# Kernel optimization log

Hardware: AMD Instinct MI355X
Metric: run time of the kernel (lower is better)

Reference implementation:

```python
import jax, jax.numpy as jnp
import numpy as np

N = 200000      # nodes
E = 12_800_000  # edges
G = 512         # graphs in batch
D = 2           # point_dim


def setup_inputs() -> dict:
    key = jax.random.key(0)
    ks = jax.random.split(key, 12)
    x = jax.random.normal(ks[0], (N, D), dtype=jnp.float32)
    edge_index = jax.random.randint(ks[1], (2, E), 0, N, dtype=jnp.int64)
    batch = jnp.sort(jax.random.randint(ks[2], (N,), 0, G, dtype=jnp.int64))
    s = 0.5
    W1 = jax.random.normal(ks[3], (D, 2), dtype=jnp.float32) * s
    b1 = jax.random.normal(ks[4], (2,), dtype=jnp.float32) * 0.1
    W2 = jax.random.normal(ks[5], (2, 2), dtype=jnp.float32) * s
    b2 = jax.random.normal(ks[6], (2,), dtype=jnp.float32) * 0.1
    W3 = jax.random.normal(ks[7], (2, 2), dtype=jnp.float32) * s
    b3 = jax.random.normal(ks[8], (2,), dtype=jnp.float32) * 0.1
    Wr = jax.random.normal(ks[9], (2, 1), dtype=jnp.float32) * s
    br = jax.random.normal(ks[10], (1,), dtype=jnp.float32) * 0.1
    return {"x": x, "edge_index": edge_index, "batch": batch,
            "W1": W1, "b1": b1, "W2": W2, "b2": b2,
            "W3": W3, "b3": b3, "Wr": Wr, "br": br}


def _gcn_conv(x, W, b, src, dst, norm, n_nodes):
    # PyG GCNConv: h = x @ W; out_i = sum_j norm_ij * h_j (incl. self-loops) + b
    h = x @ W
    agg = jax.ops.segment_sum(h[src] * norm[:, None], dst, num_segments=n_nodes)
    return agg + b


def reference(x, edge_index, batch, W1, b1, W2, b2, W3, b3, Wr, br):
    n = x.shape[0]
    loop = jnp.arange(n, dtype=edge_index.dtype)
    # GCNConv adds self-loops; same edge_index for all layers, so do it once.
    src = jnp.concatenate([edge_index[0], loop])
    dst = jnp.concatenate([edge_index[1], loop])
    # symmetric normalization: deg from target nodes (incl self-loops)
    deg = jax.ops.segment_sum(jnp.ones(dst.shape[0], x.dtype), dst, num_segments=n)
    dinv = jnp.where(deg > 0, jax.lax.rsqrt(deg), 0.0)
    norm = dinv[src] * dinv[dst]

    h = jax.nn.relu(_gcn_conv(x, W1, b1, src, dst, norm, n))
    h = jax.nn.relu(_gcn_conv(h, W2, b2, src, dst, norm, n))
    h = jax.nn.relu(_gcn_conv(h, W3, b3, src, dst, norm, n))
    pooled = jax.ops.segment_sum(h, batch, num_segments=G)  # global_add_pool -> [G, 2]
    return (pooled @ Wr + br)[:, 0]  # squeeze(1) -> [G]
```

## Files before the change

### kernel.cpp

```cpp
#include <hip/hip_runtime.h>

#define BLK 256
#define BLK2 1024
#define BSHIFT 8
#define BSIZE 256
#define NSLICE 256
#define SCAN_T 1024
#define KPAD 1024
#define EPT 8
#define TILE (BLK * EPT)
#define TILE2 (BLK2 * EPT)

typedef int iv4 __attribute__((ext_vector_type(4)));

template <typename T>
__device__ __forceinline__ T ntload(const T* p) { return __builtin_nontemporal_load(p); }

__device__ __forceinline__ iv4 ntload4(const int* p) {
    return __builtin_nontemporal_load((const iv4*)p);
}

template <int CTRL>
__device__ __forceinline__ float dpp_add(float v) {
    int t = __builtin_amdgcn_update_dpp(0, __float_as_int(v), CTRL, 0xf, 0xf, true);
    return v + __int_as_float(t);
}
__device__ __forceinline__ float wave_sum63(float v) {
    v = dpp_add<0x111>(v);
    v = dpp_add<0x112>(v);
    v = dpp_add<0x114>(v);
    v = dpp_add<0x118>(v);
    v = dpp_add<0x142>(v);
    v = dpp_add<0x143>(v);
    return v;
}


__global__ void __launch_bounds__(BLK2) k_hist(const int* __restrict__ dst,
                                               int* __restrict__ partial,
                                               int E, int chunk, int K) {
    extern __shared__ int cnt[];
    int s = blockIdx.x;
    for (int i = threadIdx.x; i < K; i += BLK2) cnt[i] = 0;
    __syncthreads();
    int lo = s * chunk, hi = min(E, lo + chunk);
    int a0 = min((lo + 3) & ~3, hi);
    int a1 = max(hi & ~3, a0);
    for (int i = lo + threadIdx.x; i < a0; i += BLK2)
        atomicAdd(&cnt[((unsigned)ntload(dst + i)) >> BSHIFT], 1);
    for (int i = a0 + 4 * threadIdx.x; i < a1; i += 4 * BLK2) {
        iv4 q = ntload4(dst + i);
        atomicAdd(&cnt[((unsigned)q.x) >> BSHIFT], 1);
        atomicAdd(&cnt[((unsigned)q.y) >> BSHIFT], 1);
        atomicAdd(&cnt[((unsigned)q.z) >> BSHIFT], 1);
        atomicAdd(&cnt[((unsigned)q.w) >> BSHIFT], 1);
    }
    for (int i = a1 + threadIdx.x; i < hi; i += BLK2)
        atomicAdd(&cnt[((unsigned)ntload(dst + i)) >> BSHIFT], 1);
    __syncthreads();
    int* prow = partial + (size_t)s * K;
    for (int i = threadIdx.x; i < K; i += BLK2) prow[i] = cnt[i];
}

__global__ void __launch_bounds__(NSLICE) k_colscan(int* __restrict__ partial,
                                                    int* __restrict__ totals, int K) {
    __shared__ int sh[NSLICE];
    int k = blockIdx.x;
    int t = threadIdx.x;
    int v = partial[(size_t)t * K + k];
    sh[t] = v;
    __syncthreads();
    for (int off = 1; off < NSLICE; off <<= 1) {
        int u = (t >= off) ? sh[t - off] : 0;
        __syncthreads();
        sh[t] += u;
        __syncthreads();
    }
    partial[(size_t)t * K + k] = sh[t] - v;
    if (t == NSLICE - 1) totals[k] = sh[t];
}

__global__ void __launch_bounds__(SCAN_T) k_base(const int* __restrict__ totals,
                                                 int* __restrict__ base, int K) {
    __shared__ int sh[SCAN_T];
    int t = threadIdx.x;
    int v = (t < K) ? totals[t] : 0;
    sh[t] = v;
    __syncthreads();
    for (int off = 1; off < SCAN_T; off <<= 1) {
        int u = (t >= off) ? sh[t - off] : 0;
        __syncthreads();
        sh[t] += u;
        __syncthreads();
    }
    if (t < K) base[t + 1] = sh[t];
    if (t == 0) base[0] = 0;
}

__global__ void __launch_bounds__(BLK2) k_scatter(const int* __restrict__ src,
                                                  const int* __restrict__ dst,
                                                  const int* __restrict__ offs,
                                                  const int* __restrict__ base,
                                                  int* __restrict__ packed,
                                                  int E, int chunk, int K, int sbits) {
    __shared__ int cnt[KPAD];
    __shared__ int cur[KPAD];
    __shared__ int gstart[KPAD];
    __shared__ int tsum[KPAD];
    __shared__ int sval[TILE2];
    __shared__ int sadr[TILE2];
    int s = blockIdx.x;
    int tid = threadIdx.x;
    const int* orow = offs + (size_t)s * K;
    cur[tid] = (tid < K) ? orow[tid] + base[tid] : 0;
    int lo = s * chunk, hi = min(E, lo + chunk);

    for (int tlo = lo; tlo < hi; tlo += TILE2) {
        cnt[tid] = 0;
        __syncthreads();

        int kk[EPT], rr[EPT], vv[EPT];
#pragma unroll
        for (int j = 0; j < EPT; ++j) {
            int i = tlo + j * BLK2 + tid;
            kk[j] = -1;
            if (i < hi) {
                int d = ntload(dst + i);
                int sc = ntload(src + i);
                kk[j] = ((unsigned)d) >> BSHIFT;
                vv[j] = ((d & (BSIZE - 1)) << sbits) | sc;
                rr[j] = atomicAdd(&cnt[kk[j]], 1);
            }
        }
        __syncthreads();

        int c = cnt[tid];
        tsum[tid] = c;
        __syncthreads();
        for (int off = 1; off < KPAD; off <<= 1) {
            int u = (tid >= off) ? tsum[tid - off] : 0;
            __syncthreads();
            tsum[tid] += u;
            __syncthreads();
        }
        int excl = tsum[tid] - c;
        gstart[tid] = cur[tid];
        cur[tid] += c;
        cnt[tid] = excl;
        __syncthreads();

#pragma unroll
        for (int j = 0; j < EPT; ++j) {
            if (kk[j] >= 0) {
                int idx = cnt[kk[j]] + rr[j];
                sval[idx] = vv[j];
                sadr[idx] = gstart[kk[j]] + rr[j];
            }
        }
        __syncthreads();

        int tot = min(hi - tlo, TILE2);
        for (int i2 = tid; i2 < tot; i2 += BLK2)
            packed[sadr[i2]] = sval[i2];
        __syncthreads();
    }
}


__global__ void __launch_bounds__(BLK) k_sort2(const int* __restrict__ packed,
                                               const int* __restrict__ base,
                                               int* __restrict__ packed2,
                                               int* __restrict__ rowptr,
                                               int sbits, int K, int E) {
    __shared__ int cnt[BSIZE];
    __shared__ int cur[BSIZE];
    __shared__ int gstart[BSIZE];
    __shared__ int sc[BLK];
    __shared__ int sval[TILE];
    __shared__ int sadr[TILE];
    int k = blockIdx.x;
    int tid = threadIdx.x;
    int lo = base[k], hi = base[k + 1];

    cnt[tid] = 0;
    __syncthreads();
    {
        int a0 = min((lo + 3) & ~3, hi);
        int a1 = max(hi & ~3, a0);
        for (int i = lo + tid; i < a0; i += BLK)
            atomicAdd(&cnt[((unsigned)ntload(packed + i)) >> sbits], 1);
        for (int i = a0 + 4 * tid; i < a1; i += 4 * BLK) {
            iv4 q = ntload4(packed + i);
            atomicAdd(&cnt[((unsigned)q.x) >> sbits], 1);
            atomicAdd(&cnt[((unsigned)q.y) >> sbits], 1);
            atomicAdd(&cnt[((unsigned)q.z) >> sbits], 1);
            atomicAdd(&cnt[((unsigned)q.w) >> sbits], 1);
        }
        for (int i = a1 + tid; i < hi; i += BLK)
            atomicAdd(&cnt[((unsigned)ntload(packed + i)) >> sbits], 1);
    }
    __syncthreads();

    int c = cnt[tid];
    sc[tid] = c;
    __syncthreads();
    for (int off = 1; off < BLK; off <<= 1) {
        int u = (tid >= off) ? sc[tid - off] : 0;
        __syncthreads();
        sc[tid] += u;
        __syncthreads();
    }
    int start = lo + sc[tid] - c;
    cur[tid] = start;
    rowptr[(k << BSHIFT) + tid] = start;
    if (k == K - 1 && tid == 0) rowptr[K << BSHIFT] = E;
    __syncthreads();

    for (int tlo = lo; tlo < hi; tlo += TILE) {
        cnt[tid] = 0;
        __syncthreads();

        int kk[EPT], rr[EPT], vv[EPT];
#pragma unroll
        for (int j = 0; j < EPT; ++j) {
            int i = tlo + j * BLK + tid;
            kk[j] = -1;
            if (i < hi) {
                int v = ntload(packed + i);
                vv[j] = v;
                kk[j] = ((unsigned)v) >> sbits;
                rr[j] = atomicAdd(&cnt[kk[j]], 1);
            }
        }
        __syncthreads();

        int d = cnt[tid];
        sc[tid] = d;
        __syncthreads();
        for (int off = 1; off < BLK; off <<= 1) {
            int u = (tid >= off) ? sc[tid - off] : 0;
            __syncthreads();
            sc[tid] += u;
            __syncthreads();
        }
        int excl = sc[tid] - d;
        gstart[tid] = cur[tid];
        cur[tid] += d;
        cnt[tid] = excl;
        __syncthreads();

#pragma unroll
        for (int j = 0; j < EPT; ++j) {
            if (kk[j] >= 0) {
                int idx = cnt[kk[j]] + rr[j];
                sval[idx] = vv[j];
                sadr[idx] = gstart[kk[j]] + rr[j];
            }
        }
        __syncthreads();

        int tot = min(hi - tlo, TILE);
        for (int i2 = tid; i2 < tot; i2 += BLK)
            packed2[sadr[i2]] = sval[i2];
        __syncthreads();
    }
}


__global__ void __launch_bounds__(BLK) k_agg4(const int* __restrict__ edges,
                                              const int* __restrict__ rowptr,
                                              const float* __restrict__ dinv,
                                              const float2* __restrict__ pin,
                                              const float* __restrict__ b,
                                              const float* __restrict__ W,
                                              float2* __restrict__ pout,
                                              int N, int smask) {
    int wid = threadIdx.x >> 6, lane = threadIdx.x & 63;
    int n = blockIdx.x * 4 + wid;
    if (n >= N) return;
    int e0 = rowptr[n], e1 = rowptr[n + 1];
    float sx = 0.f, sy = 0.f;
    for (int i = e0 + lane; i < e1; i += 64) {
        float2 e = pin[((unsigned)edges[i]) & smask];
        sx += e.x;
        sy += e.y;
    }
    sx = wave_sum63(sx);
    sy = wave_sum63(sy);
    if (lane == 63) {
        float di = dinv[n];
        float2 self = pin[n];
        float ax = sx + self.x, ay = sy + self.y;
        float h0 = fmaxf(fmaf(di, ax, b[0]), 0.f);
        float h1 = fmaxf(fmaf(di, ay, b[1]), 0.f);
        pout[n] = make_float2(di * (h0 * W[0] + h1 * W[2]),
                              di * (h0 * W[1] + h1 * W[3]));
    }
}

__global__ void __launch_bounds__(BLK) k_agg4f(const int* __restrict__ edges,
                                               const int* __restrict__ rowptr,
                                               const float* __restrict__ dinv,
                                               const float2* __restrict__ pin,
                                               const float* __restrict__ b,
                                               const float* __restrict__ Wr,
                                               float* __restrict__ sv,
                                               int N, int smask) {
    int wid = threadIdx.x >> 6, lane = threadIdx.x & 63;
    int n = blockIdx.x * 4 + wid;
    if (n >= N) return;
    int e0 = rowptr[n], e1 = rowptr[n + 1];
    float sx = 0.f, sy = 0.f;
    for (int i = e0 + lane; i < e1; i += 64) {
        float2 e = pin[((unsigned)edges[i]) & smask];
        sx += e.x;
        sy += e.y;
    }
    sx = wave_sum63(sx);
    sy = wave_sum63(sy);
    if (lane == 63) {
        float di = dinv[n];
        float2 self = pin[n];
        float ax = sx + self.x, ay = sy + self.y;
        float h0 = fmaxf(fmaf(di, ax, b[0]), 0.f);
        float h1 = fmaxf(fmaf(di, ay, b[1]), 0.f);
        sv[n] = fmaf(h0, Wr[0], h1 * Wr[1]);
    }
}


__global__ void k_node1(const int* __restrict__ rowptr, const float* __restrict__ x,
                        const float* __restrict__ W1, float* __restrict__ dinv,
                        float2* __restrict__ p1, int N) {
    int i = blockIdx.x * BLK + threadIdx.x;
    if (i >= N) return;
    int deg = rowptr[i + 1] - rowptr[i];
    float di = rsqrtf((float)deg + 1.0f);
    dinv[i] = di;
    float2 xv = ((const float2*)x)[i];
    float w00 = W1[0], w01 = W1[1], w10 = W1[2], w11 = W1[3];
    p1[i] = make_float2(di * (xv.x * w00 + xv.y * w10),
                        di * (xv.x * w01 + xv.y * w11));
}

__global__ void k_out_init(float* __restrict__ out, const float* __restrict__ br, int G) {
    int i = blockIdx.x * BLK + threadIdx.x;
    if (i < G) out[i] = br[0];
}

__global__ void k_pool(const float* __restrict__ sv, const int* __restrict__ batch,
                       float* __restrict__ out, int N) {
    int i = blockIdx.x * BLK + threadIdx.x;
    bool valid = i < N;
    float s = valid ? sv[i] : 0.f;
    int key = valid ? batch[i] : -1;
    int lane = threadIdx.x & 63;
    for (int off = 1; off < 64; off <<= 1) {
        float s2 = __shfl_down(s, off);
        int k2 = __shfl_down(key, off);
        if (lane + off < 64 && k2 == key) s += s2;
    }
    int kprev = __shfl_up(key, 1);
    if (valid && (lane == 0 || kprev != key)) unsafeAtomicAdd(&out[key], s);
}


extern "C" void kernel_launch(void* const* d_in, const int* in_sizes, int n_in,
                              void* d_out, int out_size, void* d_ws, size_t ws_size,
                              hipStream_t stream) {
    const float* x    = (const float*)d_in[0];
    const int*   ei   = (const int*)d_in[1];
    const int*   batch= (const int*)d_in[2];
    const float* W1   = (const float*)d_in[3];
    const float* b1   = (const float*)d_in[4];
    const float* W2   = (const float*)d_in[5];
    const float* b2   = (const float*)d_in[6];
    const float* W3   = (const float*)d_in[7];
    const float* b3   = (const float*)d_in[8];
    const float* Wr   = (const float*)d_in[9];
    const float* br   = (const float*)d_in[10];
    float* out = (float*)d_out;

    int N = in_sizes[0] / 2;
    int E = in_sizes[1] / 2;
    int G = out_size;
    const int* src = ei;
    const int* dst = ei + E;

    int K = (N + BSIZE - 1) >> BSHIFT;
    if (K > KPAD) return;
    int S = NSLICE;
    int chunk = (E + S - 1) / S;

    int sbits = 1;
    while ((1 << sbits) < N) ++sbits;
    if (sbits + BSHIFT > 31) return;
    int smask = (1 << sbits) - 1;

    auto pad16 = [](size_t b) { return (b + 15) & ~(size_t)15; };
    size_t need = pad16((size_t)E * 4)
                + pad16((size_t)S * K * 4)
                + pad16((size_t)(K + 1) * 4)
                + pad16((size_t)K * 4)
                + pad16((size_t)E * 4)
                + pad16(((size_t)K * BSIZE + 1) * 4)
                + pad16((size_t)N * 4)
                + 2 * pad16((size_t)N * 8)
                + pad16((size_t)N * 4);
    if (need > ws_size) return;

    char* w = (char*)d_ws;
    size_t off = 0;
    auto carve = [&](size_t bytes) { void* p = w + off; off += (bytes + 15) & ~(size_t)15; return p; };
    int*    packed  = (int*)carve((size_t)E * 4);
    int*    hpart   = (int*)carve((size_t)S * K * 4);
    int*    basep   = (int*)carve((size_t)(K + 1) * 4);
    int*    totals  = (int*)carve((size_t)K * 4);
    int*    packed2 = (int*)carve((size_t)E * 4);
    int*    rowptr  = (int*)carve(((size_t)K * BSIZE + 1) * 4);
    float*  dinv    = (float*)carve((size_t)N * 4);
    float2* pA      = (float2*)carve((size_t)N * 8);
    float2* pB      = (float2*)carve((size_t)N * 8);
    float*  sv      = (float*)carve((size_t)N * 4);

    int NB = (N + BLK - 1) / BLK;
    int GB = (G + BLK - 1) / BLK;
    int WB = (N + 3) / 4;
    size_t smemK = (size_t)K * 4;

    k_hist   <<<S, BLK2, smemK, stream>>>(dst, hpart, E, chunk, K);
    k_colscan<<<K, NSLICE, 0, stream>>>(hpart, totals, K);
    k_base   <<<1, SCAN_T, 0, stream>>>(totals, basep, K);
    k_scatter<<<S, BLK2, 0, stream>>>(src, dst, hpart, basep, packed, E, chunk, K, sbits);

    k_sort2  <<<K, BLK, 0, stream>>>(packed, basep, packed2, rowptr, sbits, K, E);

    k_node1  <<<NB, BLK, 0, stream>>>(rowptr, x, W1, dinv, pA, N);

    k_agg4   <<<WB, BLK, 0, stream>>>(packed2, rowptr, dinv, pA, b1, W2, pB, N, smask);
    k_agg4   <<<WB, BLK, 0, stream>>>(packed2, rowptr, dinv, pB, b2, W3, pA, N, smask);
    k_agg4f  <<<WB, BLK, 0, stream>>>(packed2, rowptr, dinv, pA, b3, Wr, sv, N, smask);

    k_out_init<<<GB, BLK, 0, stream>>>(out, br, G);
    k_pool    <<<NB, BLK, 0, stream>>>(sv, batch, out, N);
}
```

Baseline: 418.5 us.

## Sort each bucket in one pass fully in LDS with 1024-thread blocks

The second-level bucket sort now loads the whole bucket into registers once (up to 18 values per thread across 1024 threads) and ranks them with a single LDS histogram. It then scatters into an LDS buffer and writes the buffer out contiguously with nontemporal stores. This replaces the old two-pass scheme, which re-read the data and ran a per-tile scan with a staged scatter. Buckets larger than the capacity fall back to a global atomic scatter, which is unordered and slow. The new scheme also uses more registers and 72KB of dynamic LDS per block, which can lower occupancy.

```diff
diff --git a/kernel.cpp b/kernel.cpp
--- a/kernel.cpp
+++ b/kernel.cpp
@@ -8,8 +8,10 @@
 #define SCAN_T 1024
 #define KPAD 1024
 #define EPT 8
-#define TILE (BLK * EPT)
 #define TILE2 (BLK2 * EPT)
+#define S2BLK 1024
+#define S2CAP 18432
+#define S2MAXJ 18
 
 typedef int iv4 __attribute__((ext_vector_type(4)));
 
@@ -166,103 +168,75 @@
     }
 }
 
-
-__global__ void __launch_bounds__(BLK) k_sort2(const int* __restrict__ packed,
-                                               const int* __restrict__ base,
-                                               int* __restrict__ packed2,
-                                               int* __restrict__ rowptr,
-                                               int sbits, int K, int E) {
+__global__ void __launch_bounds__(S2BLK) k_sort2(const int* __restrict__ packed,
+                                                 const int* __restrict__ base,
+                                                 int* __restrict__ packed2,
+                                                 int* __restrict__ rowptr,
+                                                 int sbits, int K, int E) {
     __shared__ int cnt[BSIZE];
+    __shared__ int sc[BSIZE];
+    __shared__ int startsh[BSIZE];
     __shared__ int cur[BSIZE];
-    __shared__ int gstart[BSIZE];
-    __shared__ int sc[BLK];
-    __shared__ int sval[TILE];
-    __shared__ int sadr[TILE];
+    extern __shared__ int sorted[];
     int k = blockIdx.x;
     int tid = threadIdx.x;
     int lo = base[k], hi = base[k + 1];
-
-    cnt[tid] = 0;
-    __syncthreads();
-    {
-        int a0 = min((lo + 3) & ~3, hi);
-        int a1 = max(hi & ~3, a0);
-        for (int i = lo + tid; i < a0; i += BLK)
+    int len = hi - lo;
+    bool fits = (len <= S2CAP);
+
+    if (tid < BSIZE) cnt[tid] = 0;
+    __syncthreads();
+
+    int v[S2MAXJ], r[S2MAXJ];
+    if (fits) {
+#pragma unroll
+        for (int j = 0; j < S2MAXJ; ++j) {
+            int i = lo + j * S2BLK + tid;
+            r[j] = -1;
+            if (i < hi) {
+                v[j] = ntload(packed + i);
+                r[j] = atomicAdd(&cnt[((unsigned)v[j]) >> sbits], 1);
+            }
+        }
+    } else {
+        for (int i = lo + tid; i < hi; i += S2BLK)
             atomicAdd(&cnt[((unsigned)ntload(packed + i)) >> sbits], 1);
-        for (int i = a0 + 4 * tid; i < a1; i += 4 * BLK) {
-            iv4 q = ntload4(packed + i);
-            atomicAdd(&cnt[((unsigned)q.x) >> sbits], 1);
-            atomicAdd(&cnt[((unsigned)q.y) >> sbits], 1);
-            atomicAdd(&cnt[((unsigned)q.z) >> sbits], 1);
-            atomicAdd(&cnt[((unsigned)q.w) >> sbits], 1);
-        }
-        for (int i = a1 + tid; i < hi; i += BLK)
-            atomicAdd(&cnt[((unsigned)ntload(packed + i)) >> sbits], 1);
-    }
-    __syncthreads();
-
-    int c = cnt[tid];
-    sc[tid] = c;
-    __syncthreads();
-    for (int off = 1; off < BLK; off <<= 1) {
-        int u = (tid >= off) ? sc[tid - off] : 0;
-        __syncthreads();
-        sc[tid] += u;
-        __syncthreads();
-    }
-    int start = lo + sc[tid] - c;
-    cur[tid] = start;
-    rowptr[(k << BSHIFT) + tid] = start;
+    }
+    __syncthreads();
+
+    if (tid < BSIZE) sc[tid] = cnt[tid];
+    __syncthreads();
+    for (int off = 1; off < BSIZE; off <<= 1) {
+        int u = 0;
+        if (tid < BSIZE && tid >= off) u = sc[tid - off];
+        __syncthreads();
+        if (tid < BSIZE) sc[tid] += u;
+        __syncthreads();
+    }
+    if (tid < BSIZE) {
+        int st = sc[tid] - cnt[tid];
+        startsh[tid] = st;
+        cur[tid] = lo + st;
+        rowptr[(k << BSHIFT) + tid] = lo + st;
+    }
     if (k == K - 1 && tid == 0) rowptr[K << BSHIFT] = E;
     __syncthreads();
 
-    for (int tlo = lo; tlo < hi; tlo += TILE) {
-        cnt[tid] = 0;
-        __syncthreads();
-
-        int kk[EPT], rr[EPT], vv[EPT];
+    if (fits) {
 #pragma unroll
-        for (int j = 0; j < EPT; ++j) {
-            int i = tlo + j * BLK + tid;
-            kk[j] = -1;
-            if (i < hi) {
-                int v = ntload(packed + i);
-                vv[j] = v;
-                kk[j] = ((unsigned)v) >> sbits;
-                rr[j] = atomicAdd(&cnt[kk[j]], 1);
-            }
-        }
-        __syncthreads();
-
-        int d = cnt[tid];
-        sc[tid] = d;
-        __syncthreads();
-        for (int off = 1; off < BLK; off <<= 1) {
-            int u = (tid >= off) ? sc[tid - off] : 0;
-            __syncthreads();
-            sc[tid] += u;
-            __syncthreads();
-        }
-        int excl = sc[tid] - d;
-        gstart[tid] = cur[tid];
-        cur[tid] += d;
-        cnt[tid] = excl;
-        __syncthreads();
-
-#pragma unroll
-        for (int j = 0; j < EPT; ++j) {
-            if (kk[j] >= 0) {
-                int idx = cnt[kk[j]] + rr[j];
-                sval[idx] = vv[j];
-                sadr[idx] = gstart[kk[j]] + rr[j];
-            }
-        }
-        __syncthreads();
-
-        int tot = min(hi - tlo, TILE);
-        for (int i2 = tid; i2 < tot; i2 += BLK)
-            packed2[sadr[i2]] = sval[i2];
-        __syncthreads();
+        for (int j = 0; j < S2MAXJ; ++j) {
+            if (r[j] >= 0)
+                sorted[startsh[((unsigned)v[j]) >> sbits] + r[j]] = v[j];
+        }
+        __syncthreads();
+        for (int i = tid; i < len; i += S2BLK)
+            __builtin_nontemporal_store(sorted[i], packed2 + lo + i);
+    } else {
+        for (int i = lo + tid; i < hi; i += S2BLK) {
+            int val = ntload(packed + i);
+            int pos = atomicAdd(&cur[((unsigned)val) >> sbits], 1);
+            packed2[pos] = val;
+        }
     }
 }
 
@@ -433,7 +407,8 @@
     k_base   <<<1, SCAN_T, 0, stream>>>(totals, basep, K);
     k_scatter<<<S, BLK2, 0, stream>>>(src, dst, hpart, basep, packed, E, chunk, K, sbits);
 
-    k_sort2  <<<K, BLK, 0, stream>>>(packed, basep, packed2, rowptr, sbits, K, E);
+    k_sort2  <<<K, S2BLK, (size_t)S2CAP * 4, stream>>>(packed, basep, packed2, rowptr,
+                                                       sbits, K, E);
 
     k_node1  <<<NB, BLK, 0, stream>>>(rowptr, x, W1, dinv, pA, N);
 
```

New measurement: 365.2 us. -12.7%, faster.
